# Performance work log

Hardware: AMD Instinct MI355X
Metric: run time of the kernel (lower is better)

The kernel has to match this reference:

```python
import jax, jax.numpy as jnp
import numpy as np

NUM_CONN = 8

def _ein_reduce(f):
    # Einstein t-norm fold over last axis: T(a,b) = ab / (2 - (a+b-ab))
    acc = f[..., 0]
    for i in range(1, f.shape[-1]):
        b = f[..., i]
        ab = acc * b
        acc = ab / (2.0 - (acc + b - ab))
    return acc

def _coein_reduce(f):
    # Einstein t-conorm fold over last axis: S(a,b) = (a+b) / (1 + ab)
    acc = f[..., 0]
    for i in range(1, f.shape[-1]):
        b = f[..., i]
        acc = (acc + b) / (1.0 + acc * b)
    return acc

def _ddlg_layer(x, w, idx, is_train):
    # x: [B, in], idx: [out, C] int, w: [out, 4]
    feats = x[:, idx]                      # [B, out, C] gather
    ops = jnp.stack([
        jnp.min(feats, axis=-1),
        jnp.max(feats, axis=-1),
        _ein_reduce(feats),
        _coein_reduce(feats),
    ], axis=-1)                            # [B, out, 4]
    if is_train:
        prob = jax.nn.softmax(w, axis=-1)  # [out, 4]
    else:
        prob = jax.nn.one_hot(jnp.argmax(w, axis=-1), 4, dtype=x.dtype)
    return jnp.einsum('bof,of->bo', ops, prob)

def setup_inputs() -> dict:
    key = jax.random.key(0)
    ks = jax.random.split(key, 6)
    sizes = [4096, 2048, 1024, 2048, 4096]
    x = jax.random.uniform(ks[0], (4096, sizes[0]), dtype=jnp.float32)
    ws = [jax.random.normal(ks[1 + i], (sizes[i + 1], 4), dtype=jnp.float32) for i in range(4)]
    rng = np.random.default_rng(0)
    idxs = []
    for i in range(4):
        # randperm-without-replacement per output neuron
        perm = np.argsort(rng.random((sizes[i + 1], sizes[i])), axis=-1)[:, :NUM_CONN]
        idxs.append(jnp.asarray(perm, dtype=jnp.int32))
    return {
        'x': x,
        'w0': ws[0], 'w1': ws[1], 'w2': ws[2], 'w3': ws[3],
        'idx0': idxs[0], 'idx1': idxs[1], 'idx2': idxs[2], 'idx3': idxs[3],
        'is_train': 1,
    }

def reference(x, w0, w1, w2, w3, idx0, idx1, idx2, idx3, is_train):
    h = _ddlg_layer(x, w0, idx0, is_train)
    h = _ddlg_layer(h, w1, idx1, is_train)
    h = _ddlg_layer(h, w2, idx2, is_train)
    h = _ddlg_layer(h, w3, idx3, is_train)
    return h
```

## Files before the change

### kernel.cpp

```cpp
#include <hip/hip_runtime.h>
#include <hip/hip_bf16.h>


#define BATCH 4096

typedef float    f2 __attribute__((ext_vector_type(2)));
typedef _Float16 h8 __attribute__((ext_vector_type(8)));

__device__ __forceinline__ float fastrcp(float x) { return __builtin_amdgcn_rcpf(x); }

__global__ __launch_bounds__(256) void probs_k(const float* __restrict__ w0,
                                               const float* __restrict__ w1,
                                               const float* __restrict__ w2,
                                               const float* __restrict__ w3,
                                               const int* __restrict__ is_train,
                                               float4* __restrict__ probs) {
    int g = blockIdx.x * 256 + threadIdx.x;
    if (g >= 9216) return;
    const float* w; int o;
    if (g < 2048)      { w = w0; o = g; }
    else if (g < 3072) { w = w1; o = g - 2048; }
    else if (g < 5120) { w = w2; o = g - 3072; }
    else               { w = w3; o = g - 5120; }
    float wv[4];
#pragma unroll
    for (int c = 0; c < 4; ++c) wv[c] = w[(o << 2) + c];
    float p[4];
    if (*is_train) {
        float m = fmaxf(fmaxf(wv[0], wv[1]), fmaxf(wv[2], wv[3]));
        float s = 0.0f;
#pragma unroll
        for (int c = 0; c < 4; ++c) { p[c] = __expf(wv[c] - m); s += p[c]; }
        float inv = fastrcp(s);
#pragma unroll
        for (int c = 0; c < 4; ++c) p[c] *= inv;
    } else {
        int a = 0; float best = wv[0];
#pragma unroll
        for (int c = 1; c < 4; ++c) if (wv[c] > best) { best = wv[c]; a = c; }
#pragma unroll
        for (int c = 0; c < 4; ++c) p[c] = (c == a) ? 1.0f : 0.0f;
    }
    probs[g] = float4{p[0], p[1], p[2], p[3]};
}

__device__ __forceinline__ void ein_pair(const f2 v[8], f2& ein, f2& coe) {
    f2 De = v[0], Ne = 2.0f - v[0];
    f2 Nc = 1.0f + v[0], Dc = 1.0f - v[0];
#pragma unroll
    for (int c = 1; c < 8; ++c) {
        f2 x = v[c];
        De *= x;
        Ne *= (2.0f - x);
        Nc *= (1.0f + x);
        Dc *= (1.0f - x);
    }
    ein.x = (2.0f * De.x) * fastrcp(Ne.x + De.x);
    ein.y = (2.0f * De.y) * fastrcp(Ne.y + De.y);
    coe.x = (Nc.x - Dc.x) * fastrcp(Nc.x + Dc.x);
    coe.y = (Nc.y - Dc.y) * fastrcp(Nc.y + Dc.y);
}

__device__ __forceinline__ void gate8(const _Float16* __restrict__ src,
                                      const int4* __restrict__ idx,
                                      const float4* __restrict__ probs,
                                      int o, float r8[8]) {
    const int4 i0 = idx[o * 2];
    const int4 i1 = idx[o * 2 + 1];
    const float4 P = probs[o];
    h8 raw[8];
    raw[0] = *(const h8*)(src + (i0.x << 3));
    raw[1] = *(const h8*)(src + (i0.y << 3));
    raw[2] = *(const h8*)(src + (i0.z << 3));
    raw[3] = *(const h8*)(src + (i0.w << 3));
    raw[4] = *(const h8*)(src + (i1.x << 3));
    raw[5] = *(const h8*)(src + (i1.y << 3));
    raw[6] = *(const h8*)(src + (i1.z << 3));
    raw[7] = *(const h8*)(src + (i1.w << 3));

    h8 mnv = raw[0], mxv = raw[0];
#pragma unroll
    for (int c = 1; c < 8; ++c) {
        mnv = __builtin_elementwise_min(mnv, raw[c]);
        mxv = __builtin_elementwise_max(mxv, raw[c]);
    }

#pragma unroll
    for (int q = 0; q < 4; ++q) {
        f2 v[8];
#pragma unroll
        for (int c = 0; c < 8; ++c)
            v[c] = f2{(float)raw[c][2 * q], (float)raw[c][2 * q + 1]};
        f2 ein, coe;
        ein_pair(v, ein, coe);
        f2 r;
        r.x = P.x * (float)mnv[2 * q]     + P.y * (float)mxv[2 * q];
        r.y = P.x * (float)mnv[2 * q + 1] + P.y * (float)mxv[2 * q + 1];
        r += P.z * ein;
        r += P.w * coe;
        r8[2 * q]     = r.x;
        r8[2 * q + 1] = r.y;
    }
}

__device__ __forceinline__ void layer_pass(const _Float16* __restrict__ src,
                                           _Float16* __restrict__ dst,
                                           const int4* __restrict__ idx,
                                           const float4* __restrict__ probs,
                                           int o) {
    float r8[8];
    gate8(src, idx, probs, o, r8);
    h8 res;
#pragma unroll
    for (int i = 0; i < 8; ++i) res[i] = (_Float16)r8[i];
    *(h8*)(dst + (o << 3)) = res;
}

__global__ __launch_bounds__(1024) void ddlg_fused(const float* __restrict__ x,
                                                   const float4* __restrict__ probs,
                                                   const int4* __restrict__ idx0,
                                                   const int4* __restrict__ idx1,
                                                   const int4* __restrict__ idx2,
                                                   const int4* __restrict__ idx3,
                                                   float* __restrict__ out) {
    __shared__ __align__(16) _Float16 lds[49152];
    const int t  = threadIdx.x;
    const int b0 = blockIdx.x << 3;

    const _Float16* xl = lds;
    _Float16*       h0 = lds + 32768;
    _Float16*       h1 = lds;
    _Float16*       h2 = lds + 32768;

    {
        const int r = t & 7;
        const int c = t >> 3;
        const float* xrow = x + (size_t)(b0 + r) * 4096;
#pragma unroll
        for (int k = 0; k < 8; ++k) {
            const int j0 = (c << 2) + (k << 9);
            const float4 F = *(const float4*)(xrow + j0);
            lds[((j0 + 0) << 3) + r] = (_Float16)F.x;
            lds[((j0 + 1) << 3) + r] = (_Float16)F.y;
            lds[((j0 + 2) << 3) + r] = (_Float16)F.z;
            lds[((j0 + 3) << 3) + r] = (_Float16)F.w;
        }
    }
    __syncthreads();

    layer_pass(xl, h0, idx0, probs, t);
    layer_pass(xl, h0, idx0, probs, t + 1024);
    __syncthreads();

    layer_pass(h0, h1, idx1, probs + 2048, t);
    __syncthreads();

    layer_pass(h1, h2, idx2, probs + 3072, t);
    layer_pass(h1, h2, idx2, probs + 3072, t + 1024);
    __syncthreads();

#pragma unroll
    for (int p = 0; p < 4; ++p) {
        const int o = (p << 10) + t;
        float r8[8];
        gate8(h2, idx3, probs + 5120, o, r8);
#pragma unroll
        for (int b = 0; b < 8; ++b)
            out[(size_t)(b0 + b) * 4096 + o] = r8[b];
    }
}

extern "C" void kernel_launch(void* const* d_in, const int* in_sizes, int n_in,
                              void* d_out, int out_size, void* d_ws, size_t ws_size,
                              hipStream_t stream) {
    const float* x        = (const float*)d_in[0];
    const float* w0       = (const float*)d_in[1];
    const float* w1       = (const float*)d_in[2];
    const float* w2       = (const float*)d_in[3];
    const float* w3       = (const float*)d_in[4];
    const int4*  idx0     = (const int4*)d_in[5];
    const int4*  idx1     = (const int4*)d_in[6];
    const int4*  idx2     = (const int4*)d_in[7];
    const int4*  idx3     = (const int4*)d_in[8];
    const int*   is_train = (const int*)d_in[9];
    float*       out      = (float*)d_out;

    float4* probs = (float4*)d_ws;

    probs_k<<<36, 256, 0, stream>>>(w0, w1, w2, w3, is_train, probs);
    ddlg_fused<<<512, 1024, 0, stream>>>(x, probs, idx0, idx1, idx2, idx3, out);
}
```

Baseline: 185.5 us.

## Halve per-block batch to 4 rows for more resident blocks, merge reciprocals

Each block now handles 4 batch rows instead of 8, so the shared-memory tile drops to 48KB, the grid doubles to 1024 blocks, and launch bounds request more resident blocks per CU. The input load is rewritten as coalesced scalar row reads packed into a 4-wide half vector. The Einstein t-norm and t-conorm divisions share a single reciprocal of the product of the two denominators. The trade-off is that each index and prob load is amortised over fewer batch rows, so index traffic doubles, and the shared-reciprocal product could lose accuracy.

```diff
diff --git a/kernel.cpp b/kernel.cpp
--- a/kernel.cpp
+++ b/kernel.cpp
@@ -5,7 +5,7 @@
 #define BATCH 4096
 
 typedef float    f2 __attribute__((ext_vector_type(2)));
-typedef _Float16 h8 __attribute__((ext_vector_type(8)));
+typedef _Float16 h4 __attribute__((ext_vector_type(4)));
 
 __device__ __forceinline__ float fastrcp(float x) { return __builtin_amdgcn_rcpf(x); }
 
@@ -44,41 +44,24 @@
     probs[g] = float4{p[0], p[1], p[2], p[3]};
 }
 
-__device__ __forceinline__ void ein_pair(const f2 v[8], f2& ein, f2& coe) {
-    f2 De = v[0], Ne = 2.0f - v[0];
-    f2 Nc = 1.0f + v[0], Dc = 1.0f - v[0];
-#pragma unroll
-    for (int c = 1; c < 8; ++c) {
-        f2 x = v[c];
-        De *= x;
-        Ne *= (2.0f - x);
-        Nc *= (1.0f + x);
-        Dc *= (1.0f - x);
-    }
-    ein.x = (2.0f * De.x) * fastrcp(Ne.x + De.x);
-    ein.y = (2.0f * De.y) * fastrcp(Ne.y + De.y);
-    coe.x = (Nc.x - Dc.x) * fastrcp(Nc.x + Dc.x);
-    coe.y = (Nc.y - Dc.y) * fastrcp(Nc.y + Dc.y);
-}
-
-__device__ __forceinline__ void gate8(const _Float16* __restrict__ src,
+__device__ __forceinline__ void gate4(const _Float16* __restrict__ src,
                                       const int4* __restrict__ idx,
                                       const float4* __restrict__ probs,
-                                      int o, float r8[8]) {
+                                      int o, float r4[4]) {
     const int4 i0 = idx[o * 2];
     const int4 i1 = idx[o * 2 + 1];
     const float4 P = probs[o];
-    h8 raw[8];
-    raw[0] = *(const h8*)(src + (i0.x << 3));
-    raw[1] = *(const h8*)(src + (i0.y << 3));
-    raw[2] = *(const h8*)(src + (i0.z << 3));
-    raw[3] = *(const h8*)(src + (i0.w << 3));
-    raw[4] = *(const h8*)(src + (i1.x << 3));
-    raw[5] = *(const h8*)(src + (i1.y << 3));
-    raw[6] = *(const h8*)(src + (i1.z << 3));
-    raw[7] = *(const h8*)(src + (i1.w << 3));
+    h4 raw[8];
+    raw[0] = *(const h4*)(src + (i0.x << 2));
+    raw[1] = *(const h4*)(src + (i0.y << 2));
+    raw[2] = *(const h4*)(src + (i0.z << 2));
+    raw[3] = *(const h4*)(src + (i0.w << 2));
+    raw[4] = *(const h4*)(src + (i1.x << 2));
+    raw[5] = *(const h4*)(src + (i1.y << 2));
+    raw[6] = *(const h4*)(src + (i1.z << 2));
+    raw[7] = *(const h4*)(src + (i1.w << 2));
 
-    h8 mnv = raw[0], mxv = raw[0];
+    h4 mnv = raw[0], mxv = raw[0];
 #pragma unroll
     for (int c = 1; c < 8; ++c) {
         mnv = __builtin_elementwise_min(mnv, raw[c]);
@@ -86,20 +69,27 @@
     }
 
 #pragma unroll
-    for (int q = 0; q < 4; ++q) {
-        f2 v[8];
+    for (int q = 0; q < 2; ++q) {
+        f2 v0 = f2{(float)raw[0][2 * q], (float)raw[0][2 * q + 1]};
+        f2 De = v0, Ne = 2.0f - v0;
+        f2 Nc = 1.0f + v0, Dc = 1.0f - v0;
 #pragma unroll
-        for (int c = 0; c < 8; ++c)
-            v[c] = f2{(float)raw[c][2 * q], (float)raw[c][2 * q + 1]};
-        f2 ein, coe;
-        ein_pair(v, ein, coe);
-        f2 r;
-        r.x = P.x * (float)mnv[2 * q]     + P.y * (float)mxv[2 * q];
-        r.y = P.x * (float)mnv[2 * q + 1] + P.y * (float)mxv[2 * q + 1];
-        r += P.z * ein;
-        r += P.w * coe;
-        r8[2 * q]     = r.x;
-        r8[2 * q + 1] = r.y;
+        for (int c = 1; c < 8; ++c) {
+            f2 v = f2{(float)raw[c][2 * q], (float)raw[c][2 * q + 1]};
+            De *= v;
+            Ne *= (2.0f - v);
+            Nc += Nc * v;
+            Dc -= Dc * v;
+        }
+        f2 s1 = Ne + De, s2 = Nc + Dc, d1 = Nc - Dc;
+        float r0 = fastrcp(s1.x * s2.x);
+        float r1 = fastrcp(s1.y * s2.y);
+        float einx = (2.0f * De.x * s2.x) * r0;
+        float einy = (2.0f * De.y * s2.y) * r1;
+        float coex = (d1.x * s1.x) * r0;
+        float coey = (d1.y * s1.y) * r1;
+        r4[2 * q]     = P.x * (float)mnv[2 * q]     + P.y * (float)mxv[2 * q]     + P.z * einx + P.w * coex;
+        r4[2 * q + 1] = P.x * (float)mnv[2 * q + 1] + P.y * (float)mxv[2 * q + 1] + P.z * einy + P.w * coey;
     }
 }
 
@@ -108,43 +98,41 @@
                                            const int4* __restrict__ idx,
                                            const float4* __restrict__ probs,
                                            int o) {
-    float r8[8];
-    gate8(src, idx, probs, o, r8);
-    h8 res;
+    float r4[4];
+    gate4(src, idx, probs, o, r4);
+    h4 res;
 #pragma unroll
-    for (int i = 0; i < 8; ++i) res[i] = (_Float16)r8[i];
-    *(h8*)(dst + (o << 3)) = res;
+    for (int i = 0; i < 4; ++i) res[i] = (_Float16)r4[i];
+    *(h4*)(dst + (o << 2)) = res;
 }
 
-__global__ __launch_bounds__(1024) void ddlg_fused(const float* __restrict__ x,
-                                                   const float4* __restrict__ probs,
-                                                   const int4* __restrict__ idx0,
-                                                   const int4* __restrict__ idx1,
-                                                   const int4* __restrict__ idx2,
-                                                   const int4* __restrict__ idx3,
-                                                   float* __restrict__ out) {
-    __shared__ __align__(16) _Float16 lds[49152];
+__global__ __launch_bounds__(1024, 8) void ddlg_fused(const float* __restrict__ x,
+                                                      const float4* __restrict__ probs,
+                                                      const int4* __restrict__ idx0,
+                                                      const int4* __restrict__ idx1,
+                                                      const int4* __restrict__ idx2,
+                                                      const int4* __restrict__ idx3,
+                                                      float* __restrict__ out) {
+    __shared__ __align__(16) _Float16 lds[24576];
     const int t  = threadIdx.x;
-    const int b0 = blockIdx.x << 3;
+    const int b0 = blockIdx.x << 2;
 
     const _Float16* xl = lds;
-    _Float16*       h0 = lds + 32768;
+    _Float16*       h0 = lds + 16384;
     _Float16*       h1 = lds;
-    _Float16*       h2 = lds + 32768;
+    _Float16*       h2 = lds + 16384;
 
-    {
-        const int r = t & 7;
-        const int c = t >> 3;
-        const float* xrow = x + (size_t)(b0 + r) * 4096;
 #pragma unroll
-        for (int k = 0; k < 8; ++k) {
-            const int j0 = (c << 2) + (k << 9);
-            const float4 F = *(const float4*)(xrow + j0);
-            lds[((j0 + 0) << 3) + r] = (_Float16)F.x;
-            lds[((j0 + 1) << 3) + r] = (_Float16)F.y;
-            lds[((j0 + 2) << 3) + r] = (_Float16)F.z;
-            lds[((j0 + 3) << 3) + r] = (_Float16)F.w;
-        }
+    for (int c = 0; c < 4; ++c) {
+        const int j = (c << 10) + t;
+        const float v0 = x[(size_t)(b0 + 0) * 4096 + j];
+        const float v1 = x[(size_t)(b0 + 1) * 4096 + j];
+        const float v2 = x[(size_t)(b0 + 2) * 4096 + j];
+        const float v3 = x[(size_t)(b0 + 3) * 4096 + j];
+        h4 hv;
+        hv[0] = (_Float16)v0; hv[1] = (_Float16)v1;
+        hv[2] = (_Float16)v2; hv[3] = (_Float16)v3;
+        *(h4*)(lds + (j << 2)) = hv;
     }
     __syncthreads();
 
@@ -162,11 +150,11 @@
 #pragma unroll
     for (int p = 0; p < 4; ++p) {
         const int o = (p << 10) + t;
-        float r8[8];
-        gate8(h2, idx3, probs + 5120, o, r8);
+        float r4[4];
+        gate4(h2, idx3, probs + 5120, o, r4);
 #pragma unroll
-        for (int b = 0; b < 8; ++b)
-            out[(size_t)(b0 + b) * 4096 + o] = r8[b];
+        for (int b = 0; b < 4; ++b)
+            out[(size_t)(b0 + b) * 4096 + o] = r4[b];
     }
 }
 
@@ -188,5 +176,5 @@
     float4* probs = (float4*)d_ws;
 
     probs_k<<<36, 256, 0, stream>>>(w0, w1, w2, w3, is_train, probs);
-    ddlg_fused<<<512, 1024, 0, stream>>>(x, probs, idx0, idx1, idx2, idx3, out);
+    ddlg_fused<<<1024, 1024, 0, stream>>>(x, probs, idx0, idx1, idx2, idx3, out);
 }
```

Result: faster. 173.1 us (-6.7%).
